# Kernel optimization log

Measured on AMD Instinct MI355X. Metric: run time of the kernel, lower is better.

Reference implementation:

```python
import jax, jax.numpy as jnp
import numpy as np

NQ, NK, H, DH = 1024, 512, 8, 64


def setup_inputs() -> dict:
    key = jax.random.key(0)
    ks = jax.random.split(key, 8)
    b, n, d, g = 4, 4096, 1024, 4
    di = H * DH  # 512
    s = lambda fan: 1.0 / np.sqrt(fan)
    return {
        "x": jax.random.normal(ks[0], (b, n, d), jnp.float32),
        "w_qr": jax.random.normal(ks[1], (g, d), jnp.float32) * s(d),
        "w_kvr": jax.random.normal(ks[2], (g, d), jnp.float32) * s(d),
        "w_q": jax.random.normal(ks[3], (g, di, d), jnp.float32) * s(d),
        "w_kv": jax.random.normal(ks[4], (g, 2 * di, d), jnp.float32) * s(d),
        "w_out": jax.random.normal(ks[5], (g, d, di), jnp.float32) * s(di),
        "null_kv": jax.random.normal(ks[6], (2, g, H, 1, DH), jnp.float32),
        "null_token": jax.random.normal(ks[7], (1, 1, d), jnp.float32),
    }


def reference(x, w_qr, w_kvr, w_q, w_kv, w_out, null_kv, null_token):
    b, n, d = x.shape
    g = w_qr.shape[0]
    bidx = jnp.arange(b)[:, None, None]
    # --- routing: per-expert token scores, top-k select (router reference) ---
    q_logits = jnp.einsum("bnd,gd->bgn", x, w_qr)
    q_top, q_idx = jax.lax.top_k(q_logits, NQ)            # [b,g,NQ]
    q_scores = jax.nn.sigmoid(q_top)[..., None]           # [b,g,NQ,1]
    queries = x[bidx, q_idx]                              # [b,g,NQ,d]
    kv_logits = jnp.einsum("bnd,gd->bgn", x, w_kvr)
    kv_top, kv_idx = jax.lax.top_k(kv_logits, NK)
    kv_scores = jax.nn.sigmoid(kv_top)[:, :, None, :, None]  # [b,g,1,NK,1]
    key_values = x[bidx, kv_idx]                          # [b,g,NK,d]
    # --- grouped attention (1x1 grouped convs == per-group matmuls) ---
    q = jnp.einsum("bgnd,ged->bgne", queries, w_q)
    kv = jnp.einsum("bgnd,ged->bgne", key_values, w_kv)
    k, v = jnp.split(kv, 2, axis=-1)
    heads = lambda t: t.reshape(b, g, -1, H, DH).transpose(0, 1, 3, 2, 4)  # b g h n dh
    q, k, v = heads(q), heads(k), heads(v)
    v = v * kv_scores                                     # values_scale
    nk = jnp.broadcast_to(null_kv[0][None], (b, g, H, 1, DH))
    nv = jnp.broadcast_to(null_kv[1][None], (b, g, H, 1, DH))
    k = jnp.concatenate([nk, k], axis=-2)
    v = jnp.concatenate([nv, v], axis=-2)
    attn = jax.nn.softmax(jnp.einsum("bghid,bghjd->bghij", q, k) * DH ** -0.5, axis=-1)
    o = jnp.einsum("bghij,bghjd->bghid", attn, v)
    o = o.transpose(0, 1, 3, 2, 4).reshape(b, g, NQ, H * DH)
    o = jnp.einsum("bgne,gde->bgnd", o, w_out)
    o = o * q_scores
    # --- scatter-add back with count normalization ---
    flat_idx = q_idx.reshape(b, g * NQ)
    flat_o = o.reshape(b, g * NQ, d)
    b2 = jnp.arange(b)[:, None]
    summed = jnp.zeros_like(x).at[b2, flat_idx].add(flat_o)
    counts = jnp.zeros((b, n), x.dtype).at[b2, flat_idx].add(1.0)[..., None]
    meaned = summed / jnp.clip(counts, 1e-5)
    return jnp.where(counts > 0, meaned, null_token)
```

## Files before the change

kernel.cpp:

```cpp
#include <hip/hip_runtime.h>
#include <math.h>

#define NB 4
#define SEQ 4096
#define DM 1024
#define NG 4
#define DI 512
#define NQS 1024
#define NKS 512
#define NHD 8
#define DHD 64
#define VTS 520

typedef unsigned int u32;
typedef unsigned short u16;
typedef __bf16 bf16x8 __attribute__((ext_vector_type(8)));
typedef float f32x4 __attribute__((ext_vector_type(4)));

__device__ __forceinline__ float bf2f(u16 u) { return __uint_as_float(((u32)u) << 16); }
__device__ __forceinline__ u16 f2bf(float f) {
  u32 u = __float_as_uint(f);
  u32 r = (u + 0x7FFFu + ((u >> 16) & 1u)) >> 16;
  return (u16)r;
}
__device__ __forceinline__ u16 f2bfh(float f) {
  union { __bf16 b; u16 u; } cv;
  cv.b = (__bf16)f;
  return cv.u;
}

__global__ __launch_bounds__(256) void router_kernel(
    const float* __restrict__ x, const float* __restrict__ wqr,
    const float* __restrict__ wkvr, float* __restrict__ qlog,
    float* __restrict__ kvlog, u16* __restrict__ xbf) {
  int tid = threadIdx.x;
  int base = blockIdx.x * 8 + (tid >> 6) * 2;
  int lane = tid & 63;
  int b = base >> 12, tok = base & 4095;
  const float4* xr0 = (const float4*)(x + ((size_t)(b * SEQ + tok)) * DM);
  const float4* xr1 = xr0 + 256;
  float4 xv0[4], xv1[4];
#pragma unroll
  for (int i = 0; i < 4; i++) {
    xv0[i] = xr0[i * 64 + lane];
    xv1[i] = xr1[i * 64 + lane];
  }
  ushort4* xrow0 = (ushort4*)(xbf + ((size_t)(b * SEQ + tok)) * DM);
  ushort4* xrow1 = xrow0 + 256;
#pragma unroll
  for (int i = 0; i < 4; i++) {
    ushort4 o0, o1;
    o0.x = f2bf(xv0[i].x); o0.y = f2bf(xv0[i].y);
    o0.z = f2bf(xv0[i].z); o0.w = f2bf(xv0[i].w);
    o1.x = f2bf(xv1[i].x); o1.y = f2bf(xv1[i].y);
    o1.z = f2bf(xv1[i].z); o1.w = f2bf(xv1[i].w);
    xrow0[i * 64 + lane] = o0;
    xrow1[i * 64 + lane] = o1;
  }
  float a0[8], a1[8];
#pragma unroll
  for (int r = 0; r < 8; r++) {
    const float4* wr =
        (const float4*)(r < 4 ? wqr + (r << 10) : wkvr + ((r - 4) << 10));
    float s0 = 0.f, s1 = 0.f;
#pragma unroll
    for (int i = 0; i < 4; i++) {
      float4 w4 = wr[i * 64 + lane];
      s0 += xv0[i].x * w4.x + xv0[i].y * w4.y + xv0[i].z * w4.z + xv0[i].w * w4.w;
      s1 += xv1[i].x * w4.x + xv1[i].y * w4.y + xv1[i].z * w4.z + xv1[i].w * w4.w;
    }
    a0[r] = s0; a1[r] = s1;
  }
#pragma unroll
  for (int r = 0; r < 8; r++) {
#pragma unroll
    for (int off = 32; off >= 1; off >>= 1) {
      a0[r] += __shfl_xor(a0[r], off);
      a1[r] += __shfl_xor(a1[r], off);
    }
    if (lane == 0) {
      if (r < 4) {
        qlog[((b << 2) | r) * SEQ + tok] = a0[r];
        qlog[((b << 2) | r) * SEQ + tok + 1] = a1[r];
      } else {
        kvlog[((b << 2) | (r - 4)) * SEQ + tok] = a0[r];
        kvlog[((b << 2) | (r - 4)) * SEQ + tok + 1] = a1[r];
      }
    }
  }
}

__global__ __launch_bounds__(256) void topk_kernel(
    const float* __restrict__ qlog, const float* __restrict__ kvlog,
    int* __restrict__ qidx, float* __restrict__ qscore,
    int* __restrict__ kvidx, float* __restrict__ kvscore,
    int* __restrict__ qpos, const float* __restrict__ wq,
    const float* __restrict__ wkv, const float* __restrict__ wout,
    u16* __restrict__ wqbf, u16* __restrict__ wkvbf, u16* __restrict__ woutbf) {
  int tid = threadIdx.x;
  if (blockIdx.x >= 32) {
    int cid = blockIdx.x - 32;
#pragma unroll
    for (int j = 0; j < 4; j++) {
      int idx = cid * 1024 + j * 256 + tid;
      const float* src; u16* dst; int off;
      if (idx < 524288)        { src = wq;   dst = wqbf;   off = idx; }
      else if (idx < 1572864)  { src = wkv;  dst = wkvbf;  off = idx - 524288; }
      else                     { src = wout; dst = woutbf; off = idx - 1572864; }
      float4 v = ((const float4*)src)[off];
      ushort4 o;
      o.x = f2bf(v.x); o.y = f2bf(v.y); o.z = f2bf(v.z); o.w = f2bf(v.w);
      ((ushort4*)dst)[off] = o;
    }
    return;
  }
  __shared__ u32 keys[4096];
  __shared__ int eqlist[2048];
  __shared__ int scnt[12];
  __shared__ int s_gt, s_eq;
  int which = blockIdx.x >> 4;
  int bg = blockIdx.x & 15;
  int K = (which == 0) ? NQS : NKS;
  const float* L = ((which == 0) ? qlog : kvlog) + bg * 4096;
  int* out_idx = ((which == 0) ? qidx : kvidx) + bg * K;
  float* out_score = ((which == 0) ? qscore : kvscore) + bg * K;
  int* qposb = qpos + bg * 4096;
  for (int e = tid; e < 4096; e += 256) {
    u32 u = __float_as_uint(L[e]);
    keys[e] = (u >> 31) ? ~u : (u | 0x80000000u);
  }
  if (which == 0)
    for (int e = tid; e < 4096; e += 256) qposb[e] = -1;
  if (tid == 0) { s_gt = 0; s_eq = 0; }
  __syncthreads();
  u32 prefix = 0;
  int remaining = K;
  for (int bit = 30; bit >= 12; bit -= 2) {
    u32 maskhi = (bit >= 30) ? 0u : (0xFFFFFFFFu << (bit + 2));
    int c3 = 0, c2 = 0, c1 = 0;
    for (int e = tid; e < 4096; e += 256) {
      u32 k = keys[e];
      if ((k & maskhi) == prefix) {
        u32 bkt = (k >> bit) & 3u;
        c3 += (bkt == 3u); c2 += (bkt == 2u); c1 += (bkt == 1u);
      }
    }
#pragma unroll
    for (int off = 32; off >= 1; off >>= 1) {
      c3 += __shfl_xor(c3, off);
      c2 += __shfl_xor(c2, off);
      c1 += __shfl_xor(c1, off);
    }
    if ((tid & 63) == 0) {
      int wv = tid >> 6;
      scnt[wv * 3 + 0] = c3; scnt[wv * 3 + 1] = c2; scnt[wv * 3 + 2] = c1;
    }
    __syncthreads();
    int n3 = scnt[0] + scnt[3] + scnt[6] + scnt[9];
    int n2 = scnt[1] + scnt[4] + scnt[7] + scnt[10];
    int n1 = scnt[2] + scnt[5] + scnt[8] + scnt[11];
    if (n3 >= remaining) prefix |= 3u << bit;
    else if (n3 + n2 >= remaining) { prefix |= 2u << bit; remaining -= n3; }
    else if (n3 + n2 + n1 >= remaining) { prefix |= 1u << bit; remaining -= n3 + n2; }
    else remaining -= (n3 + n2 + n1);
    __syncthreads();
  }
  u32 T = prefix;
  for (int e = tid; e < 4096; e += 256) {
    u32 k = keys[e];
    u32 k20 = k & 0xFFFFF000u;
    if (k20 > T) {
      int pos = atomicAdd(&s_gt, 1);
      out_idx[pos] = e;
      u32 uo = (k >> 31) ? (k & 0x7FFFFFFFu) : ~k;
      float v = __uint_as_float(uo);
      out_score[pos] = 1.0f / (1.0f + __expf(-v));
      if (which == 0) qposb[e] = pos;
    } else if (k20 == T) {
      int p = atomicAdd(&s_eq, 1);
      if (p < 2048) eqlist[p] = e;
    }
  }
  __syncthreads();
  int gt = s_gt;
  int eq = min(s_eq, 2048);
  int need = K - gt;
  for (int i = tid; i < eq; i += 256) {
    int my = eqlist[i];
    u32 myk = keys[my];
    int rank = 0;
    for (int j = 0; j < eq; j++) {
      u32 kj = keys[eqlist[j]];
      rank += (kj > myk || (kj == myk && eqlist[j] < my)) ? 1 : 0;
    }
    if (rank < need) {
      int pos = gt + rank;
      out_idx[pos] = my;
      u32 uo = (myk >> 31) ? (myk & 0x7FFFFFFFu) : ~myk;
      float v = __uint_as_float(uo);
      out_score[pos] = 1.0f / (1.0f + __expf(-v));
      if (which == 0) qposb[my] = pos;
    }
  }
}

struct Ptr4 { const u16* p[4]; };

__device__ __forceinline__ void stage_tile(const Ptr4& A, const Ptr4& B,
                                           u16* Asmb, u16* Bsmb, int kt, int w) {
#pragma unroll
  for (int r = 0; r < 4; r++) {
    char* ldsA = (char*)Asmb + (r * 256 + w * 64) * 16;
    __builtin_amdgcn_global_load_lds(
        (const __attribute__((address_space(1))) void*)(A.p[r] + kt * 64),
        (__attribute__((address_space(3))) void*)ldsA, 16, 0, 0);
  }
#pragma unroll
  for (int r = 0; r < 4; r++) {
    char* ldsB = (char*)Bsmb + (r * 256 + w * 64) * 16;
    __builtin_amdgcn_global_load_lds(
        (const __attribute__((address_space(1))) void*)(B.p[r] + kt * 64),
        (__attribute__((address_space(3))) void*)ldsB, 16, 0, 0);
  }
}

__device__ __forceinline__ void mfma_core(Ptr4 A, Ptr4 B, u16* Asm0, u16* Bsm0,
                                          u16* Asm1, u16* Bsm1, int ktiles,
                                          int tid, f32x4 (&acc)[4][4]) {
  int w = tid >> 6, lane = tid & 63;
  int col = lane & 15, quad = lane >> 4;
  int wr = w >> 1, wc = w & 1;
  stage_tile(A, B, Asm0, Bsm0, 0, w);
  __syncthreads();
  for (int kt = 0; kt < ktiles; kt++) {
    const u16* Ac = (kt & 1) ? Asm1 : Asm0;
    const u16* Bc = (kt & 1) ? Bsm1 : Bsm0;
    if (kt + 1 < ktiles)
      stage_tile(A, B, (kt & 1) ? Asm0 : Asm1, (kt & 1) ? Bsm0 : Bsm1, kt + 1, w);
#pragma unroll
    for (int k04 = 0; k04 < 8; k04 += 4) {
      bf16x8 af[4], bfr[4];
#pragma unroll
      for (int t = 0; t < 4; t++) {
        int rowa = wr * 64 + t * 16 + col;
        int sp = (quad + k04) ^ (col & 7);
        af[t] = *(const bf16x8*)((const char*)Ac + (rowa * 8 + sp) * 16);
        int rowb = wc * 64 + t * 16 + col;
        bfr[t] = *(const bf16x8*)((const char*)Bc + (rowb * 8 + sp) * 16);
      }
#pragma unroll
      for (int t = 0; t < 4; t++)
#pragma unroll
        for (int u = 0; u < 4; u++)
          acc[t][u] = __builtin_amdgcn_mfma_f32_16x16x32_bf16(af[t], bfr[u], acc[t][u], 0, 0, 0);
    }
    __syncthreads();
  }
}

__global__ __launch_bounds__(256) void gemm_qkvproj(
    const u16* __restrict__ xbf, const int* __restrict__ qidx,
    const int* __restrict__ kvidx, const u16* __restrict__ wqbf,
    const u16* __restrict__ wkvbf, const float* __restrict__ kvscore,
    u16* __restrict__ qbuf, u16* __restrict__ kbuf, u16* __restrict__ vtbuf) {
  __shared__ __align__(16) u16 Asm[2][8192], Bsm[2][8192];
  __shared__ int ridx[128];
  int tid = threadIdx.x;
  int id = blockIdx.x;
  bool is_q = (id & 1) == 0;
  int sid = id >> 1;
  int bg = sid >> 5, r5 = sid & 31;
  int b = bg >> 2, g = bg & 3;
  int w = tid >> 6, lane = tid & 63;
  int col = lane & 15, quad = lane >> 4;
  int wr = w >> 1, wc = w & 1;

  if (is_q) {
    int col0 = (r5 & 3) * 128, row0 = (r5 >> 2) * 128;
    if (tid < 128) ridx[tid] = qidx[bg * NQS + row0 + tid];
    __syncthreads();
    Ptr4 A, B;
#pragma unroll
    for (int r = 0; r < 4; r++) {
      int G = r * 256 + tid;
      int row = G >> 3;
      int seg = (G & 7) ^ (row & 7);
      A.p[r] = xbf + ((size_t)b * SEQ + ridx[row]) * DM + seg * 8;
      B.p[r] = wqbf + ((size_t)g * DI + col0 + row) * DM + seg * 8;
    }
    f32x4 acc[4][4] = {};
    mfma_core(A, B, Asm[0], Bsm[0], Asm[1], Bsm[1], DM / 64, tid, acc);
#pragma unroll
    for (int t = 0; t < 4; t++)
#pragma unroll
      for (int u = 0; u < 4; u++)
#pragma unroll
        for (int r = 0; r < 4; r++) {
          int rowg = row0 + wr * 64 + t * 16 + quad * 4 + r;
          int colg = col0 + wc * 64 + u * 16 + col;
          qbuf[((size_t)bg * NQS + rowg) * DI + colg] = f2bf(acc[t][u][r] * 0.125f);
        }
  } else {
    int col0 = (r5 & 7) * 128, row0 = (r5 >> 3) * 128;
    if (tid < 128) ridx[tid] = kvidx[bg * NKS + row0 + tid];
    __syncthreads();
    Ptr4 A, B;
#pragma unroll
    for (int r = 0; r < 4; r++) {
      int G = r * 256 + tid;
      int row = G >> 3;
      int seg = (G & 7) ^ (row & 7);
      A.p[r] = xbf + ((size_t)b * SEQ + ridx[row]) * DM + seg * 8;
      B.p[r] = wkvbf + ((size_t)g * (2 * DI) + col0 + row) * DM + seg * 8;
    }
    f32x4 acc[4][4] = {};
    mfma_core(A, B, Asm[0], Bsm[0], Asm[1], Bsm[1], DM / 64, tid, acc);
    if (col0 < DI) {
#pragma unroll
      for (int t = 0; t < 4; t++)
#pragma unroll
        for (int u = 0; u < 4; u++)
#pragma unroll
          for (int r = 0; r < 4; r++) {
            int rowg = row0 + wr * 64 + t * 16 + quad * 4 + r;
            int colg = col0 + wc * 64 + u * 16 + col;
            kbuf[((size_t)bg * NKS + rowg) * DI + colg] = f2bf(acc[t][u][r]);
          }
    } else {
#pragma unroll
      for (int t = 0; t < 4; t++) {
        int base = row0 + wr * 64 + t * 16 + quad * 4;
        float sc0 = kvscore[bg * NKS + base + 0];
        float sc1 = kvscore[bg * NKS + base + 1];
        float sc2 = kvscore[bg * NKS + base + 2];
        float sc3 = kvscore[bg * NKS + base + 3];
#pragma unroll
        for (int u = 0; u < 4; u++) {
          int vc = col0 - DI + wc * 64 + u * 16 + col;
          int h = vc >> 6, d = vc & 63;
          u32 lo = (u32)f2bf(acc[t][u][0] * sc0) | ((u32)f2bf(acc[t][u][1] * sc1) << 16);
          u32 hi = (u32)f2bf(acc[t][u][2] * sc2) | ((u32)f2bf(acc[t][u][3] * sc3) << 16);
          *(uint2*)&vtbuf[(((size_t)bg * NHD + h) * DHD + d) * VTS + base] =
              make_uint2(lo, hi);
        }
      }
    }
  }
}

__global__ __launch_bounds__(256) void gemm_outproj(
    const u16* __restrict__ obuf, const u16* __restrict__ woutbf,
    const float* __restrict__ qscore, u16* __restrict__ oproj_lo,
    u16* __restrict__ oproj_hi) {
  int bg = blockIdx.z, g = bg & 3;
  int row0 = blockIdx.y * 128, col0 = blockIdx.x * 128;
  __shared__ __align__(16) u16 Asm[2][8192], Bsm[2][8192];
  int tid = threadIdx.x;
  Ptr4 A, B;
#pragma unroll
  for (int r = 0; r < 4; r++) {
    int G = r * 256 + tid;
    int row = G >> 3;
    int seg = (G & 7) ^ (row & 7);
    A.p[r] = obuf + ((size_t)bg * NQS + row0 + row) * DI + seg * 8;
    B.p[r] = woutbf + ((size_t)g * DM + col0 + row) * DI + seg * 8;
  }
  f32x4 acc[4][4] = {};
  mfma_core(A, B, Asm[0], Bsm[0], Asm[1], Bsm[1], DI / 64, tid, acc);
  int w = tid >> 6, lane = tid & 63;
  int col = lane & 15, quad = lane >> 4;
  int wr = w >> 1, wc = w & 1;
  u16* obase = (bg < 8 ? oproj_lo : oproj_hi) + (size_t)(bg & 7) * NQS * DM;
#pragma unroll
  for (int t = 0; t < 4; t++)
#pragma unroll
    for (int r = 0; r < 4; r++) {
      int rowg = row0 + wr * 64 + t * 16 + quad * 4 + r;
      float sc = qscore[bg * NQS + rowg];
      u16* orow = obase + (size_t)rowg * DM;
#pragma unroll
      for (int u = 0; u < 4; u++) {
        int colg = col0 + wc * 64 + u * 16 + col;
        orow[colg] = f2bfh(acc[t][u][r] * sc);
      }
    }
}

__global__ __launch_bounds__(256) void finalize_gather(
    const u16* __restrict__ oproj_lo, const u16* __restrict__ oproj_hi,
    const int* __restrict__ qpos, const float* __restrict__ null_token,
    float* __restrict__ dout) {
  int blk = blockIdx.x;
  int b = blk >> 12;
  int tok = blk & 4095;
  int tid = threadIdx.x;
  const u16* obase = (b < 2) ? oproj_lo : oproj_hi;
  int zoff = (b & 1) * 4;
  float4 acc = {0.f, 0.f, 0.f, 0.f};
  int cnt = 0;
#pragma unroll
  for (int g = 0; g < 4; g++) {
    int pos = qpos[(((b << 2) | g)) * 4096 + tok];
    if (pos >= 0) {
      const uint2* row =
          (const uint2*)(obase + ((size_t)(zoff + g) * NQS + pos) * DM);
      uint2 v = row[tid];
      acc.x += bf2f((u16)(v.x & 0xFFFF));
      acc.y += bf2f((u16)(v.x >> 16));
      acc.z += bf2f((u16)(v.y & 0xFFFF));
      acc.w += bf2f((u16)(v.y >> 16));
      cnt++;
    }
  }
  float4* dst = (float4*)(dout + ((size_t)b * SEQ + tok) * DM) + tid;
  if (cnt > 0) {
    float inv = 1.0f / cnt;
    acc.x *= inv; acc.y *= inv; acc.z *= inv; acc.w *= inv;
    *dst = acc;
  } else {
    *dst = ((const float4*)null_token)[tid];
  }
}

__global__ __launch_bounds__(256, 4) void attn_mfma(
    const u16* __restrict__ qbuf, const u16* __restrict__ kbuf,
    const u16* __restrict__ vtbuf, const float* __restrict__ null_kv,
    u16* __restrict__ obuf) {
  int id = blockIdx.x;
  int qt = id >> 7;
  int h = id & 7;
  int bg = (id >> 3) & 15;
  int g = bg & 3;
  int tid = threadIdx.x;
  int w = tid >> 6, lane = tid & 63;
  int col = lane & 15, quad = lane >> 4;

  __shared__ __align__(16) u16 Ks[64][72];
  __shared__ __align__(16) u16 Vts[64][72];
  __shared__ __align__(16) u16 Ps[4][32][72];

  int q0 = qt * 128 + w * 32;
  const u16* qp0 = qbuf + ((size_t)bg * NQS + q0 + col) * DI + h * DHD + quad * 8;
  bf16x8 qa[2][2];
  qa[0][0] = *(const bf16x8*)qp0;
  qa[0][1] = *(const bf16x8*)(qp0 + 32);
  qa[1][0] = *(const bf16x8*)(qp0 + 16 * DI);
  qa[1][1] = *(const bf16x8*)(qp0 + 16 * DI + 32);

  const float* kn = null_kv + ((size_t)(0 * NG + g) * NHD + h) * DHD;
  const float* vn = null_kv + ((size_t)(1 * NG + g) * NHD + h) * DHD;
  float m_run[2], l_lane[2];
  f32x4 oacc[2][4];
#pragma unroll
  for (int s = 0; s < 2; s++) {
    float sn = 0.f;
#pragma unroll
    for (int i = 0; i < 8; i++) {
      sn += (float)qa[s][0][i] * kn[quad * 8 + i];
      sn += (float)qa[s][1][i] * kn[32 + quad * 8 + i];
    }
    sn += __shfl_xor(sn, 16);
    sn += __shfl_xor(sn, 32);
    m_run[s] = sn;
    l_lane[s] = (quad == 0) ? 1.f : 0.f;
  }
#pragma unroll
  for (int t = 0; t < 4; t++) {
    float v = vn[t * 16 + col];
    f32x4 tmp = {v, v, v, v};
    oacc[0][t] = tmp;
    oacc[1][t] = tmp;
  }

  int sr = tid >> 2, ss = tid & 3;
  const u16* kptr = kbuf + ((size_t)bg * NKS + sr) * DI + h * DHD + ss * 16;
  const u16* vptr = vtbuf + (((size_t)bg * NHD + h) * DHD + sr) * VTS + ss * 16;
  uint4* kdst = (uint4*)&Ks[sr][ss * 16];
  uint4* vdst = (uint4*)&Vts[sr][ss * 16];
  uint4 ck0, ck1, cv0, cv1;
  { const uint4* p = (const uint4*)kptr; ck0 = p[0]; ck1 = p[1]; }
  { const uint4* p = (const uint4*)vptr; cv0 = p[0]; cv1 = p[1]; }

  for (int c = 0; c < 8; ++c) {
    kdst[0] = ck0; kdst[1] = ck1;
    vdst[0] = cv0; vdst[1] = cv1;
    if (c < 7) {
      const uint4* p = (const uint4*)(kptr + (size_t)(c + 1) * 64 * DI);
      ck0 = p[0]; ck1 = p[1];
      const uint4* q4 = (const uint4*)(vptr + (c + 1) * 64);
      cv0 = q4[0]; cv1 = q4[1];
    }
    __syncthreads();

    f32x4 sv[2][4];
#pragma unroll
    for (int t = 0; t < 4; t++) {
      bf16x8 kb0 = *(const bf16x8*)&Ks[t * 16 + col][quad * 8];
      bf16x8 kb1 = *(const bf16x8*)&Ks[t * 16 + col][quad * 8 + 32];
      f32x4 z = {0.f, 0.f, 0.f, 0.f};
      f32x4 s0 = __builtin_amdgcn_mfma_f32_16x16x32_bf16(kb0, qa[0][0], z, 0, 0, 0);
      sv[0][t] = __builtin_amdgcn_mfma_f32_16x16x32_bf16(kb1, qa[0][1], s0, 0, 0, 0);
      f32x4 s1 = __builtin_amdgcn_mfma_f32_16x16x32_bf16(kb0, qa[1][0], z, 0, 0, 0);
      sv[1][t] = __builtin_amdgcn_mfma_f32_16x16x32_bf16(kb1, qa[1][1], s1, 0, 0, 0);
    }

#pragma unroll
    for (int s = 0; s < 2; s++) {
      float pm = sv[s][0][0];
#pragma unroll
      for (int t = 0; t < 4; t++)
#pragma unroll
        for (int r = 0; r < 4; r++) pm = fmaxf(pm, sv[s][t][r]);
      pm = fmaxf(pm, __shfl_xor(pm, 16));
      pm = fmaxf(pm, __shfl_xor(pm, 32));
      if (!__all(pm <= m_run[s] + 8.0f)) {
        float mnew = fmaxf(m_run[s], pm);
        float alpha = __expf(m_run[s] - mnew);
        m_run[s] = mnew;
        l_lane[s] *= alpha;
#pragma unroll
        for (int r = 0; r < 4; r++) {
          float a_o = __shfl(alpha, quad * 4 + r);
#pragma unroll
          for (int t = 0; t < 4; t++) oacc[s][t][r] *= a_o;
        }
      }
      float rs = 0.f;
#pragma unroll
      for (int t = 0; t < 4; t++) {
        float p0 = __expf(sv[s][t][0] - m_run[s]);
        float p1 = __expf(sv[s][t][1] - m_run[s]);
        float p2 = __expf(sv[s][t][2] - m_run[s]);
        float p3 = __expf(sv[s][t][3] - m_run[s]);
        rs += (p0 + p1) + (p2 + p3);
        u32 lo = (u32)f2bfh(p0) | ((u32)f2bfh(p1) << 16);
        u32 hi = (u32)f2bfh(p2) | ((u32)f2bfh(p3) << 16);
        *(uint2*)&Ps[w][s * 16 + col][t * 16 + quad * 4] = make_uint2(lo, hi);
      }
      l_lane[s] += rs;
    }

#pragma unroll
    for (int s2 = 0; s2 < 2; s2++) {
      bf16x8 pa0 = *(const bf16x8*)&Ps[w][col][s2 * 32 + quad * 8];
      bf16x8 pa1 = *(const bf16x8*)&Ps[w][16 + col][s2 * 32 + quad * 8];
#pragma unroll
      for (int t = 0; t < 4; t++) {
        bf16x8 vb = *(const bf16x8*)&Vts[t * 16 + col][s2 * 32 + quad * 8];
        oacc[0][t] = __builtin_amdgcn_mfma_f32_16x16x32_bf16(pa0, vb, oacc[0][t], 0, 0, 0);
        oacc[1][t] = __builtin_amdgcn_mfma_f32_16x16x32_bf16(pa1, vb, oacc[1][t], 0, 0, 0);
      }
    }
    __syncthreads();
  }

#pragma unroll
  for (int s = 0; s < 2; s++) {
    float l = l_lane[s];
    l += __shfl_xor(l, 16);
    l += __shfl_xor(l, 32);
    float inv = 1.0f / l;
#pragma unroll
    for (int r = 0; r < 4; r++) {
      float ir = __shfl(inv, quad * 4 + r);
#pragma unroll
      for (int t = 0; t < 4; t++) {
        obuf[((size_t)bg * NQS + q0 + s * 16 + quad * 4 + r) * DI + h * DHD +
             t * 16 + col] = f2bfh(oacc[s][t][r] * ir);
      }
    }
  }
}

extern "C" void kernel_launch(void* const* d_in, const int* in_sizes, int n_in,
                              void* d_out, int out_size, void* d_ws, size_t ws_size,
                              hipStream_t stream) {
  const float* x = (const float*)d_in[0];
  const float* wqr = (const float*)d_in[1];
  const float* wkvr = (const float*)d_in[2];
  const float* wq = (const float*)d_in[3];
  const float* wkv = (const float*)d_in[4];
  const float* wout = (const float*)d_in[5];
  const float* nullkv = (const float*)d_in[6];
  const float* nulltok = (const float*)d_in[7];
  float* out = (float*)d_out;
  char* ws = (char*)d_ws;
  float* qlog = (float*)(ws + 0);
  float* kvlog = (float*)(ws + 262144);
  int* qidx = (int*)(ws + 524288);
  int* kvidx = (int*)(ws + 589824);
  float* qscore = (float*)(ws + 622592);
  float* kvscore = (float*)(ws + 688128);
  u16* qbuf = (u16*)(ws + 786432);
  u16* kbuf = (u16*)(ws + 17563648);
  u16* vtbuf = (u16*)(ws + 25952256);
  u16* obuf = (u16*)(ws + 34476032);
  u16* xbf = (u16*)(ws + 51253248);
  u16* wqbf = (u16*)(ws + 84807680);
  u16* wkvbf = (u16*)(ws + 89001984);
  u16* woutbf = (u16*)(ws + 97390592);
  int* qpos = (int*)(ws + 0);
  u16* oproj_lo = (u16*)(ws + 786432);
  u16* oproj_hi = (u16*)(ws + 51253248);

  router_kernel<<<2048, 256, 0, stream>>>(x, wqr, wkvr, qlog, kvlog, xbf);
  topk_kernel<<<2080, 256, 0, stream>>>(qlog, kvlog, qidx, qscore, kvidx,
                                        kvscore, qpos, wq, wkv, wout, wqbf,
                                        wkvbf, woutbf);
  gemm_qkvproj<<<1024, 256, 0, stream>>>(xbf, qidx, kvidx, wqbf, wkvbf, kvscore,
                                         qbuf, kbuf, vtbuf);
  attn_mfma<<<1024, 256, 0, stream>>>(qbuf, kbuf, vtbuf, nullkv, obuf);
  gemm_outproj<<<dim3(8, 8, 16), 256, 0, stream>>>(obuf, woutbf, qscore,
                                                   oproj_lo, oproj_hi);
  finalize_gather<<<16384, 256, 0, stream>>>(oproj_lo, oproj_hi, qpos, nulltok,
                                             out);
}
```

Measured before the change: 294.8 us.

## Use 8-wave 512-thread blocks for projection GEMMs with 2x4 warp tiling

Both projection GEMM kernels move from 4 waves per block (each computing a 64x64 sub-tile) to 8 waves (each computing 64x32), keeping the 128x128 block tile. Tile staging is split so every thread issues two A and two B loads per k-step instead of four of each. The goal is more waves per CU to hide latency and less work and fewer registers per wave. The cost is more B-fragment LDS reads per unit of MFMA work and heavier barrier synchronisation across 8 waves.

```diff
diff --git a/kernel.cpp b/kernel.cpp
--- a/kernel.cpp
+++ b/kernel.cpp
@@ -204,61 +204,62 @@
   }
 }
 
-struct Ptr4 { const u16* p[4]; };
-
-__device__ __forceinline__ void stage_tile(const Ptr4& A, const Ptr4& B,
-                                           u16* Asmb, u16* Bsmb, int kt, int w) {
-#pragma unroll
-  for (int r = 0; r < 4; r++) {
-    char* ldsA = (char*)Asmb + (r * 256 + w * 64) * 16;
+struct Ptr2 { const u16* a[2]; const u16* b[2]; };
+
+__device__ __forceinline__ void stage_tile512(const Ptr2& P, u16* Asmb,
+                                              u16* Bsmb, int kt, int w) {
+#pragma unroll
+  for (int r = 0; r < 2; r++) {
+    char* ldsA = (char*)Asmb + (r * 512 + w * 64) * 16;
     __builtin_amdgcn_global_load_lds(
-        (const __attribute__((address_space(1))) void*)(A.p[r] + kt * 64),
+        (const __attribute__((address_space(1))) void*)(P.a[r] + kt * 64),
         (__attribute__((address_space(3))) void*)ldsA, 16, 0, 0);
-  }
-#pragma unroll
-  for (int r = 0; r < 4; r++) {
-    char* ldsB = (char*)Bsmb + (r * 256 + w * 64) * 16;
+    char* ldsB = (char*)Bsmb + (r * 512 + w * 64) * 16;
     __builtin_amdgcn_global_load_lds(
-        (const __attribute__((address_space(1))) void*)(B.p[r] + kt * 64),
+        (const __attribute__((address_space(1))) void*)(P.b[r] + kt * 64),
         (__attribute__((address_space(3))) void*)ldsB, 16, 0, 0);
   }
 }
 
-__device__ __forceinline__ void mfma_core(Ptr4 A, Ptr4 B, u16* Asm0, u16* Bsm0,
-                                          u16* Asm1, u16* Bsm1, int ktiles,
-                                          int tid, f32x4 (&acc)[4][4]) {
+__device__ __forceinline__ void mfma_core512(Ptr2 P, u16* Asm0, u16* Bsm0,
+                                             u16* Asm1, u16* Bsm1, int ktiles,
+                                             int tid, f32x4 (&acc)[4][2]) {
   int w = tid >> 6, lane = tid & 63;
   int col = lane & 15, quad = lane >> 4;
-  int wr = w >> 1, wc = w & 1;
-  stage_tile(A, B, Asm0, Bsm0, 0, w);
+  int wr = w >> 2, wc = w & 3;
+  stage_tile512(P, Asm0, Bsm0, 0, w);
   __syncthreads();
   for (int kt = 0; kt < ktiles; kt++) {
     const u16* Ac = (kt & 1) ? Asm1 : Asm0;
     const u16* Bc = (kt & 1) ? Bsm1 : Bsm0;
     if (kt + 1 < ktiles)
-      stage_tile(A, B, (kt & 1) ? Asm0 : Asm1, (kt & 1) ? Bsm0 : Bsm1, kt + 1, w);
+      stage_tile512(P, (kt & 1) ? Asm0 : Asm1, (kt & 1) ? Bsm0 : Bsm1, kt + 1, w);
 #pragma unroll
     for (int k04 = 0; k04 < 8; k04 += 4) {
-      bf16x8 af[4], bfr[4];
+      bf16x8 af[4], bfr[2];
 #pragma unroll
       for (int t = 0; t < 4; t++) {
         int rowa = wr * 64 + t * 16 + col;
         int sp = (quad + k04) ^ (col & 7);
         af[t] = *(const bf16x8*)((const char*)Ac + (rowa * 8 + sp) * 16);
-        int rowb = wc * 64 + t * 16 + col;
-        bfr[t] = *(const bf16x8*)((const char*)Bc + (rowb * 8 + sp) * 16);
+      }
+#pragma unroll
+      for (int u = 0; u < 2; u++) {
+        int rowb = wc * 32 + u * 16 + col;
+        int sp = (quad + k04) ^ (col & 7);
+        bfr[u] = *(const bf16x8*)((const char*)Bc + (rowb * 8 + sp) * 16);
       }
 #pragma unroll
       for (int t = 0; t < 4; t++)
 #pragma unroll
-        for (int u = 0; u < 4; u++)
+        for (int u = 0; u < 2; u++)
           acc[t][u] = __builtin_amdgcn_mfma_f32_16x16x32_bf16(af[t], bfr[u], acc[t][u], 0, 0, 0);
     }
     __syncthreads();
   }
 }
 
-__global__ __launch_bounds__(256) void gemm_qkvproj(
+__global__ __launch_bounds__(512) void gemm_qkvproj(
     const u16* __restrict__ xbf, const int* __restrict__ qidx,
     const int* __restrict__ kvidx, const u16* __restrict__ wqbf,
     const u16* __restrict__ wkvbf, const float* __restrict__ kvscore,
@@ -273,57 +274,57 @@
   int b = bg >> 2, g = bg & 3;
   int w = tid >> 6, lane = tid & 63;
   int col = lane & 15, quad = lane >> 4;
-  int wr = w >> 1, wc = w & 1;
+  int wr = w >> 2, wc = w & 3;
 
   if (is_q) {
     int col0 = (r5 & 3) * 128, row0 = (r5 >> 2) * 128;
     if (tid < 128) ridx[tid] = qidx[bg * NQS + row0 + tid];
     __syncthreads();
-    Ptr4 A, B;
-#pragma unroll
-    for (int r = 0; r < 4; r++) {
-      int G = r * 256 + tid;
+    Ptr2 P;
+#pragma unroll
+    for (int r = 0; r < 2; r++) {
+      int G = r * 512 + tid;
       int row = G >> 3;
       int seg = (G & 7) ^ (row & 7);
-      A.p[r] = xbf + ((size_t)b * SEQ + ridx[row]) * DM + seg * 8;
-      B.p[r] = wqbf + ((size_t)g * DI + col0 + row) * DM + seg * 8;
-    }
-    f32x4 acc[4][4] = {};
-    mfma_core(A, B, Asm[0], Bsm[0], Asm[1], Bsm[1], DM / 64, tid, acc);
+      P.a[r] = xbf + ((size_t)b * SEQ + ridx[row]) * DM + seg * 8;
+      P.b[r] = wqbf + ((size_t)g * DI + col0 + row) * DM + seg * 8;
+    }
+    f32x4 acc[4][2] = {};
+    mfma_core512(P, Asm[0], Bsm[0], Asm[1], Bsm[1], DM / 64, tid, acc);
 #pragma unroll
     for (int t = 0; t < 4; t++)
 #pragma unroll
-      for (int u = 0; u < 4; u++)
+      for (int u = 0; u < 2; u++)
 #pragma unroll
         for (int r = 0; r < 4; r++) {
           int rowg = row0 + wr * 64 + t * 16 + quad * 4 + r;
-          int colg = col0 + wc * 64 + u * 16 + col;
+          int colg = col0 + wc * 32 + u * 16 + col;
           qbuf[((size_t)bg * NQS + rowg) * DI + colg] = f2bf(acc[t][u][r] * 0.125f);
         }
   } else {
     int col0 = (r5 & 7) * 128, row0 = (r5 >> 3) * 128;
     if (tid < 128) ridx[tid] = kvidx[bg * NKS + row0 + tid];
     __syncthreads();
-    Ptr4 A, B;
-#pragma unroll
-    for (int r = 0; r < 4; r++) {
-      int G = r * 256 + tid;
+    Ptr2 P;
+#pragma unroll
+    for (int r = 0; r < 2; r++) {
+      int G = r * 512 + tid;
       int row = G >> 3;
       int seg = (G & 7) ^ (row & 7);
-      A.p[r] = xbf + ((size_t)b * SEQ + ridx[row]) * DM + seg * 8;
-      B.p[r] = wkvbf + ((size_t)g * (2 * DI) + col0 + row) * DM + seg * 8;
-    }
-    f32x4 acc[4][4] = {};
-    mfma_core(A, B, Asm[0], Bsm[0], Asm[1], Bsm[1], DM / 64, tid, acc);
+      P.a[r] = xbf + ((size_t)b * SEQ + ridx[row]) * DM + seg * 8;
+      P.b[r] = wkvbf + ((size_t)g * (2 * DI) + col0 + row) * DM + seg * 8;
+    }
+    f32x4 acc[4][2] = {};
+    mfma_core512(P, Asm[0], Bsm[0], Asm[1], Bsm[1], DM / 64, tid, acc);
     if (col0 < DI) {
 #pragma unroll
       for (int t = 0; t < 4; t++)
 #pragma unroll
-        for (int u = 0; u < 4; u++)
+        for (int u = 0; u < 2; u++)
 #pragma unroll
           for (int r = 0; r < 4; r++) {
             int rowg = row0 + wr * 64 + t * 16 + quad * 4 + r;
-            int colg = col0 + wc * 64 + u * 16 + col;
+            int colg = col0 + wc * 32 + u * 16 + col;
             kbuf[((size_t)bg * NKS + rowg) * DI + colg] = f2bf(acc[t][u][r]);
           }
     } else {
@@ -335,8 +336,8 @@
         float sc2 = kvscore[bg * NKS + base + 2];
         float sc3 = kvscore[bg * NKS + base + 3];
 #pragma unroll
-        for (int u = 0; u < 4; u++) {
-          int vc = col0 - DI + wc * 64 + u * 16 + col;
+        for (int u = 0; u < 2; u++) {
+          int vc = col0 - DI + wc * 32 + u * 16 + col;
           int h = vc >> 6, d = vc & 63;
           u32 lo = (u32)f2bf(acc[t][u][0] * sc0) | ((u32)f2bf(acc[t][u][1] * sc1) << 16);
           u32 hi = (u32)f2bf(acc[t][u][2] * sc2) | ((u32)f2bf(acc[t][u][3] * sc3) << 16);
@@ -348,7 +349,7 @@
   }
 }
 
-__global__ __launch_bounds__(256) void gemm_outproj(
+__global__ __launch_bounds__(512) void gemm_outproj(
     const u16* __restrict__ obuf, const u16* __restrict__ woutbf,
     const float* __restrict__ qscore, u16* __restrict__ oproj_lo,
     u16* __restrict__ oproj_hi) {
@@ -356,20 +357,20 @@
   int row0 = blockIdx.y * 128, col0 = blockIdx.x * 128;
   __shared__ __align__(16) u16 Asm[2][8192], Bsm[2][8192];
   int tid = threadIdx.x;
-  Ptr4 A, B;
-#pragma unroll
-  for (int r = 0; r < 4; r++) {
-    int G = r * 256 + tid;
+  Ptr2 P;
+#pragma unroll
+  for (int r = 0; r < 2; r++) {
+    int G = r * 512 + tid;
     int row = G >> 3;
     int seg = (G & 7) ^ (row & 7);
-    A.p[r] = obuf + ((size_t)bg * NQS + row0 + row) * DI + seg * 8;
-    B.p[r] = woutbf + ((size_t)g * DM + col0 + row) * DI + seg * 8;
-  }
-  f32x4 acc[4][4] = {};
-  mfma_core(A, B, Asm[0], Bsm[0], Asm[1], Bsm[1], DI / 64, tid, acc);
+    P.a[r] = obuf + ((size_t)bg * NQS + row0 + row) * DI + seg * 8;
+    P.b[r] = woutbf + ((size_t)g * DM + col0 + row) * DI + seg * 8;
+  }
+  f32x4 acc[4][2] = {};
+  mfma_core512(P, Asm[0], Bsm[0], Asm[1], Bsm[1], DI / 64, tid, acc);
   int w = tid >> 6, lane = tid & 63;
   int col = lane & 15, quad = lane >> 4;
-  int wr = w >> 1, wc = w & 1;
+  int wr = w >> 2, wc = w & 3;
   u16* obase = (bg < 8 ? oproj_lo : oproj_hi) + (size_t)(bg & 7) * NQS * DM;
 #pragma unroll
   for (int t = 0; t < 4; t++)
@@ -379,8 +380,8 @@
       float sc = qscore[bg * NQS + rowg];
       u16* orow = obase + (size_t)rowg * DM;
 #pragma unroll
-      for (int u = 0; u < 4; u++) {
-        int colg = col0 + wc * 64 + u * 16 + col;
+      for (int u = 0; u < 2; u++) {
+        int colg = col0 + wc * 32 + u * 16 + col;
         orow[colg] = f2bfh(acc[t][u][r] * sc);
       }
     }
@@ -607,10 +608,10 @@
   topk_kernel<<<2080, 256, 0, stream>>>(qlog, kvlog, qidx, qscore, kvidx,
                                         kvscore, qpos, wq, wkv, wout, wqbf,
                                         wkvbf, woutbf);
-  gemm_qkvproj<<<1024, 256, 0, stream>>>(xbf, qidx, kvidx, wqbf, wkvbf, kvscore,
+  gemm_qkvproj<<<1024, 512, 0, stream>>>(xbf, qidx, kvidx, wqbf, wkvbf, kvscore,
                                          qbuf, kbuf, vtbuf);
   attn_mfma<<<1024, 256, 0, stream>>>(qbuf, kbuf, vtbuf, nullkv, obuf);
-  gemm_outproj<<<dim3(8, 8, 16), 256, 0, stream>>>(obuf, woutbf, qscore,
+  gemm_outproj<<<dim3(8, 8, 16), 512, 0, stream>>>(obuf, woutbf, qscore,
                                                    oproj_lo, oproj_hi);
   finalize_gather<<<16384, 256, 0, stream>>>(oproj_lo, oproj_hi, qpos, nulltok,
                                              out);
```

After: 295.6 us. Within noise of the previous version (+0.3%).
